# Kernel optimization log

Hardware: AMD Instinct MI355X
Metric: run time of the kernel (lower is better)

The kernel has to match this reference:

```python
import jax, jax.numpy as jnp
import numpy as np

B, S, D, H = 4, 2048, 1024, 16
DK = D // H
SCALE = 1.0 / np.float32(np.sqrt(DK))


def setup_inputs() -> dict:
    key = jax.random.key(0)
    ks = jax.random.split(key, 11)
    w = lambda k: (jax.random.normal(k, (D, D), jnp.float32) * 0.02)
    b = lambda k: (jax.random.normal(k, (D,), jnp.float32) * 0.02)
    return {
        "Q": jax.random.normal(ks[0], (B, S, D), jnp.float32),
        "K": jax.random.normal(ks[1], (B, S, D), jnp.float32),
        "V": jax.random.normal(ks[2], (B, S, D), jnp.float32),
        "Wq": w(ks[3]), "bq": b(ks[4]),
        "Wk": w(ks[5]), "bk": b(ks[6]),
        "Wv": w(ks[7]), "bv": b(ks[8]),
        "Wo": w(ks[9]), "bo": b(ks[10]),
        # causal mask, broadcast over batch and heads: [1,1,S,S]
        "mask": jnp.tril(jnp.ones((1, 1, S, S), dtype=bool)),
    }


def reference(Q, K, V, Wq, bq, Wk, bk, Wv, bv, Wo, bo, mask):
    def proj(x, W, bias):
        # [B,S,D] -> [B,H,S,DK]
        return (x @ W + bias).reshape(B, S, H, DK).transpose(0, 2, 1, 3)

    q = proj(Q, Wq, bq)
    k = proj(K, Wk, bk)
    v = proj(V, Wv, bv)
    scores = jnp.einsum("bhqd,bhkd->bhqk", q, k) * SCALE  # [B,H,S,S]
    scores = jnp.where(mask, scores, jnp.float32(-1e9))
    attn = jax.nn.softmax(scores, axis=-1)
    out = jnp.einsum("bhqk,bhkd->bhqd", attn, v)  # [B,H,S,DK]
    out = out.transpose(0, 2, 1, 3).reshape(B, S, D)
    return out @ Wo + bo
```

## Files before the change

kernel.cpp:

```cpp
#include <hip/hip_runtime.h>
#include <hip/hip_bf16.h>
#include <stdint.h>

#define BB 4
#define SS 2048
#define DD 1024
#define HH 16
#define DKK 64
#define MM (BB * SS)

typedef __hip_bfloat16 bf16;
typedef __attribute__((ext_vector_type(8))) short frag8;
typedef __attribute__((ext_vector_type(4))) float f32x4;

#define GLDS16(g, l)                                                        \
  __builtin_amdgcn_global_load_lds(                                         \
      (const __attribute__((address_space(1))) void*)(g),                   \
      (__attribute__((address_space(3))) void*)(l), 16, 0, 0)

#define MFMA __builtin_amdgcn_mfma_f32_16x16x32_bf16

__device__ __forceinline__ unsigned short f2bu(float f) {
  __hip_bfloat16 h = __float2bfloat16(f);
  return *reinterpret_cast<unsigned short*>(&h);
}

struct WtArgs {
  const float* s[3];
  unsigned short* d[3];
};
__global__ __launch_bounds__(256) void wtrans_kernel(WtArgs a) {
  const float* __restrict__ W = a.s[blockIdx.z];
  unsigned short* __restrict__ Wt = a.d[blockIdx.z];
  __shared__ float t[64][68];
  const int n0 = blockIdx.x * 64, k0 = blockIdx.y * 64;
  const int tid = threadIdx.x;
#pragma unroll
  for (int it = 0; it < 4; ++it) {
    const int kk = it * 16 + (tid >> 4);
    const int nn = (tid & 15) * 4;
    const float4 v = *(const float4*)&W[(size_t)(k0 + kk) * DD + n0 + nn];
    *(float4*)&t[kk][nn] = v;
  }
  __syncthreads();
#pragma unroll
  for (int it = 0; it < 2; ++it) {
    const int n = it * 32 + (tid >> 3);
    const int c = tid & 7;
    frag8 pk;
#pragma unroll
    for (int j = 0; j < 8; ++j) pk[j] = (short)f2bu(t[c * 8 + j][n]);
    *(frag8*)&Wt[(size_t)(n0 + n) * DD + k0 + c * 8] = pk;
  }
}

struct CvtArgs {
  const float* s[3];
  unsigned short* d[3];
};
__global__ __launch_bounds__(256) void cvt_kernel(CvtArgs a) {
  const float* __restrict__ src = a.s[blockIdx.y];
  unsigned short* __restrict__ dst = a.d[blockIdx.y];
  const size_t i = ((size_t)blockIdx.x * 256 + threadIdx.x) * 8;
  const float4 v0 = *(const float4*)&src[i];
  const float4 v1 = *(const float4*)&src[i + 4];
  frag8 pk;
  pk[0] = (short)f2bu(v0.x); pk[1] = (short)f2bu(v0.y);
  pk[2] = (short)f2bu(v0.z); pk[3] = (short)f2bu(v0.w);
  pk[4] = (short)f2bu(v1.x); pk[5] = (short)f2bu(v1.y);
  pk[6] = (short)f2bu(v1.z); pk[7] = (short)f2bu(v1.w);
  *(frag8*)&dst[i] = pk;
}

struct GArgs {
  const void* A[3];
  const unsigned short* W[3];
  const float* bias[3];
  void* out[3];
  float oscale[3];
  int abf16[3];
  int omode[3];
};

__global__ __launch_bounds__(256) void gemm32_kernel(GArgs ga) {
  constexpr int K = DD;
  const int z = blockIdx.z;
  const unsigned short* __restrict__ A = (const unsigned short*)ga.A[z];
  const unsigned short* __restrict__ Wt = ga.W[z];
  const float* __restrict__ bias = ga.bias[z];
  void* __restrict__ outv = ga.out[z];
  const float oscale = ga.oscale[z];
  const int omode = ga.omode[z];

  __shared__ unsigned short As[2][128 * 32];
  __shared__ unsigned short Bs[2][128 * 32];
  const int tid = threadIdx.x;
  const int wave = tid >> 6, lane = tid & 63, quad = lane >> 4, l15 = lane & 15;
  const int wr = wave >> 1, wc = wave & 1;
  const int mt = blockIdx.x * 8 + (blockIdx.y >> 3);
  const int nt = blockIdx.y & 7;
  const int m0 = mt * 128, n0 = nt * 128;

  f32x4 acc[4][4] = {};

  auto stage = [&](int buf, int k0) {
#pragma unroll
    for (int j = 0; j < 2; ++j) {
      const int win = wave * 2 + j;
      const int srl = lane >> 3;
      const int pp = lane & 7;
      const int p = pp ^ srl;
      const int row = (win * 8 + srl) * 2 + (p >> 2);
      const int c = p & 3;
      const unsigned off = __builtin_amdgcn_readfirstlane(
          (unsigned)(buf * 8192 + win * 1024));
      GLDS16(&A[(size_t)(m0 + row) * K + k0 + c * 8], (char*)&As[0][0] + off);
      GLDS16(&Wt[(size_t)(n0 + row) * K + k0 + c * 8], (char*)&Bs[0][0] + off);
    }
  };
  auto compute = [&](int buf) {
    frag8 af[4], bfr[4];
#pragma unroll
    for (int mi = 0; mi < 4; ++mi) {
      const int R = wr * 64 + mi * 16 + l15;
      const int sr = R >> 1;
      const int pp = (((R & 1) << 2) | quad) ^ (sr & 7);
      af[mi] = *(const frag8*)&As[buf][sr * 64 + pp * 8];
    }
#pragma unroll
    for (int ni = 0; ni < 4; ++ni) {
      const int R = wc * 64 + ni * 16 + l15;
      const int sr = R >> 1;
      const int pp = (((R & 1) << 2) | quad) ^ (sr & 7);
      bfr[ni] = *(const frag8*)&Bs[buf][sr * 64 + pp * 8];
    }
#pragma unroll
    for (int mi = 0; mi < 4; ++mi)
#pragma unroll
      for (int ni = 0; ni < 4; ++ni)
        acc[mi][ni] = MFMA(af[mi], bfr[ni], acc[mi][ni], 0, 0, 0);
  };

  stage(0, 0);
  __syncthreads();
#pragma unroll 1
  for (int t = 0; t < 32; ++t) {
    if (t + 1 < 32) stage((t & 1) ^ 1, (t + 1) * 32);
    compute(t & 1);
    __syncthreads();
  }

#pragma unroll
  for (int mi = 0; mi < 4; ++mi) {
#pragma unroll
    for (int ni = 0; ni < 4; ++ni) {
#pragma unroll
      for (int r = 0; r < 4; ++r) {
        const int grow = m0 + wr * 64 + mi * 16 + quad * 4 + r;
        const int gcol = n0 + wc * 64 + ni * 16 + l15;
        const float val = (acc[mi][ni][r] + bias[gcol]) * oscale;
        if (omode == 2) {
          ((float*)outv)[(size_t)grow * DD + gcol] = val;
        } else {
          const int b = grow / SS, s = grow % SS;
          const int h = gcol / DKK, dk = gcol % DKK;
          unsigned short* outp = (unsigned short*)outv;
          if (omode == 0)
            outp[(((size_t)(b * HH + h)) * SS + s) * DKK + dk] = f2bu(val);
          else
            outp[(((size_t)(b * HH + h)) * DKK + dk) * SS + s] = f2bu(val);
        }
      }
    }
  }
}

__global__ __launch_bounds__(256) void gemm_kernel(GArgs ga) {
  constexpr int K = DD;
  const int z = blockIdx.z;
  const void* __restrict__ Av = ga.A[z];
  const unsigned short* __restrict__ Wt = ga.W[z];
  const float* __restrict__ bias = ga.bias[z];
  void* __restrict__ outv = ga.out[z];
  const float oscale = ga.oscale[z];
  const int abf = ga.abf16[z];
  const int omode = ga.omode[z];

  __shared__ unsigned short Bs[2][128 * 64];
  __shared__ unsigned short As[2][128 * 64];
  const int tid = threadIdx.x;
  const int wave = tid >> 6, lane = tid & 63, quad = lane >> 4, l15 = lane & 15;
  const int wr = wave >> 1, wc = wave & 1;
  const int mt = blockIdx.x * 8 + (blockIdx.y >> 3);
  const int nt = blockIdx.y & 7;
  const int m0 = mt * 128, n0 = nt * 128;

  f32x4 acc[4][4] = {};
  float4 r0[4], r1[4];

  auto stageB = [&](int buf, int k0) {
#pragma unroll
    for (int c = 0; c < 4; ++c) {
      const int row = c * 32 + wave * 8 + (lane >> 3);
      const int gc = ((lane & 7) ^ (row & 7)) * 8;
      const unsigned short* g = &Wt[(size_t)(n0 + row) * K + k0 + gc];
      unsigned off = __builtin_amdgcn_readfirstlane(
          (unsigned)(buf * 16384 + (c * 32 + wave * 8) * 128));
      GLDS16(g, (char*)&Bs[0][0] + off);
    }
  };
  auto stageA16 = [&](int buf, int k0) {
    const unsigned short* Ap = (const unsigned short*)Av;
#pragma unroll
    for (int c = 0; c < 4; ++c) {
      const int row = c * 32 + wave * 8 + (lane >> 3);
      const int gc = ((lane & 7) ^ (row & 7)) * 8;
      const unsigned short* g = &Ap[(size_t)(m0 + row) * K + k0 + gc];
      unsigned off = __builtin_amdgcn_readfirstlane(
          (unsigned)(buf * 16384 + (c * 32 + wave * 8) * 128));
      GLDS16(g, (char*)&As[0][0] + off);
    }
  };
  auto loadA32 = [&](int k0) {
    const float* Ap = (const float*)Av;
#pragma unroll
    for (int it = 0; it < 4; ++it) {
      const int row = it * 32 + (tid >> 3);
      const int c = tid & 7;
      r0[it] = *(const float4*)&Ap[(size_t)(m0 + row) * K + k0 + c * 8];
      r1[it] = *(const float4*)&Ap[(size_t)(m0 + row) * K + k0 + c * 8 + 4];
    }
  };
  auto writeA32 = [&](int buf) {
#pragma unroll
    for (int it = 0; it < 4; ++it) {
      const int row = it * 32 + (tid >> 3);
      const int c = tid & 7;
      frag8 pk;
      pk[0] = (short)f2bu(r0[it].x); pk[1] = (short)f2bu(r0[it].y);
      pk[2] = (short)f2bu(r0[it].z); pk[3] = (short)f2bu(r0[it].w);
      pk[4] = (short)f2bu(r1[it].x); pk[5] = (short)f2bu(r1[it].y);
      pk[6] = (short)f2bu(r1[it].z); pk[7] = (short)f2bu(r1[it].w);
      *(frag8*)&As[buf][row * 64 + ((c ^ (row & 7)) * 8)] = pk;
    }
  };
  auto compute = [&](int buf) {
#pragma unroll
    for (int s = 0; s < 2; ++s) {
      frag8 a2[4], b2[4];
#pragma unroll
      for (int mi = 0; mi < 4; ++mi)
        a2[mi] = *(const frag8*)&As[buf][(wr * 64 + mi * 16 + l15) * 64 +
                                         (((s * 4 + quad) ^ (l15 & 7)) * 8)];
#pragma unroll
      for (int ni = 0; ni < 4; ++ni)
        b2[ni] = *(const frag8*)&Bs[buf][(wc * 64 + ni * 16 + l15) * 64 +
                                         (((s * 4 + quad) ^ (l15 & 7)) * 8)];
#pragma unroll
      for (int mi = 0; mi < 4; ++mi)
#pragma unroll
        for (int ni = 0; ni < 4; ++ni)
          acc[mi][ni] = MFMA(a2[mi], b2[ni], acc[mi][ni], 0, 0, 0);
    }
  };

  if (abf) {
    stageB(0, 0);
    stageA16(0, 0);
  } else {
    loadA32(0);
    stageB(0, 0);
    writeA32(0);
  }
  __syncthreads();

#pragma unroll 1
  for (int t = 0; t < 16; t += 2) {
    if (t + 1 < 16) {
      if (abf) {
        stageB(1, (t + 1) * 64);
        stageA16(1, (t + 1) * 64);
      } else {
        loadA32((t + 1) * 64);
        stageB(1, (t + 1) * 64);
      }
    }
    compute(0);
    if (!abf && t + 1 < 16) writeA32(1);
    __syncthreads();
    if (t + 2 < 16) {
      if (abf) {
        stageB(0, (t + 2) * 64);
        stageA16(0, (t + 2) * 64);
      } else {
        loadA32((t + 2) * 64);
        stageB(0, (t + 2) * 64);
      }
    }
    compute(1);
    if (!abf && t + 2 < 16) writeA32(0);
    __syncthreads();
  }

#pragma unroll
  for (int mi = 0; mi < 4; ++mi) {
#pragma unroll
    for (int ni = 0; ni < 4; ++ni) {
#pragma unroll
      for (int r = 0; r < 4; ++r) {
        const int grow = m0 + wr * 64 + mi * 16 + quad * 4 + r;
        const int gcol = n0 + wc * 64 + ni * 16 + l15;
        const float val = (acc[mi][ni][r] + bias[gcol]) * oscale;
        if (omode == 2) {
          ((float*)outv)[(size_t)grow * DD + gcol] = val;
        } else {
          const int b = grow / SS, s = grow % SS;
          const int h = gcol / DKK, dk = gcol % DKK;
          unsigned short* outp = (unsigned short*)outv;
          if (omode == 0)
            outp[(((size_t)(b * HH + h)) * SS + s) * DKK + dk] = f2bu(val);
          else
            outp[(((size_t)(b * HH + h)) * DKK + dk) * SS + s] = f2bu(val);
        }
      }
    }
  }
}

__global__ __launch_bounds__(512) void fattn_kernel(
    const unsigned short* __restrict__ q, const unsigned short* __restrict__ k,
    const unsigned short* __restrict__ vt, unsigned short* __restrict__ ctx) {
  __shared__ unsigned short Ks[2][64 * 64];
  __shared__ unsigned short Vs[2][64 * 64];
  __shared__ unsigned short P_lds[8][16][36];
  const int tid = threadIdx.x;
  const int wave = tid >> 6, lane = tid & 63, quad = lane >> 4, l15 = lane & 15;
  const int bh = blockIdx.x & 63;
  const int tp = blockIdx.x >> 6;
  const size_t qkb = (size_t)bh * SS * DKK;
  const size_t vtb = (size_t)bh * DKK * SS;
  const int b = bh / HH, h = bh % HH;

  frag8 ones;
#pragma unroll
  for (int s = 0; s < 8; ++s) ones[s] = (short)0x3F80;

  auto stage = [&](int buf, int jt) {
    const int row = wave * 8 + (lane >> 3);
    const int gc = ((lane & 7) ^ (lane >> 3)) * 8;
    const unsigned off =
        __builtin_amdgcn_readfirstlane((unsigned)(buf * 8192 + wave * 1024));
    GLDS16(&k[qkb + (size_t)(jt * 64 + row) * DKK + gc],
           (char*)&Ks[0][0] + off);
    GLDS16(&vt[vtb + (size_t)row * SS + jt * 64 + gc], (char*)&Vs[0][0] + off);
  };

  for (int half = 0; half < 2; ++half) {
    const int t = half ? (15 - tp) : tp;
    const int q0 = t * 128 + wave * 16;

    const frag8 aq0 =
        *(const frag8*)&q[qkb + (size_t)(q0 + l15) * DKK + quad * 8];
    const frag8 aq1 =
        *(const frag8*)&q[qkb + (size_t)(q0 + l15) * DKK + 32 + quad * 8];

    f32x4 oacc[4] = {};
    f32x4 lacc = {};

    const int nT = 2 * t + 2;
    stage(0, 0);
    __syncthreads();

    for (int jt = 0; jt < nT; ++jt) {
      const int p = jt & 1;
      if (jt + 1 < nT) stage(1 - p, jt + 1);
      const bool allmask = jt * 64 > q0 + 15;
      const bool anymask = jt * 64 + 63 > q0;

      if (!allmask) {
#pragma unroll
        for (int jsub = 0; jsub < 2; ++jsub) {
          f32x4 sc[2];
#pragma unroll
          for (int g = 0; g < 2; ++g) {
            const int row = jsub * 32 + g * 16 + l15;
            const frag8 kf0 =
                *(const frag8*)&Ks[p][row * 64 + ((quad ^ (l15 & 7)) * 8)];
            const frag8 kf1 =
                *(const frag8*)&Ks[p][row * 64 + (((4 + quad) ^ (l15 & 7)) * 8)];
            f32x4 z = {};
            z = MFMA(aq0, kf0, z, 0, 0, 0);
            sc[g] = MFMA(aq1, kf1, z, 0, 0, 0);
          }
          float p0[4], p1[4];
          if (anymask) {
            const int jg = jt * 64 + jsub * 32;
#pragma unroll
            for (int r = 0; r < 4; ++r) {
              const int ig = q0 + quad * 4 + r;
              p0[r] = (jg + l15 <= ig) ? __expf(sc[0][r]) : 0.f;
              p1[r] = (jg + 16 + l15 <= ig) ? __expf(sc[1][r]) : 0.f;
            }
          } else {
#pragma unroll
            for (int r = 0; r < 4; ++r) {
              p0[r] = __expf(sc[0][r]);
              p1[r] = __expf(sc[1][r]);
            }
          }
#pragma unroll
          for (int r = 0; r < 4; ++r) {
            P_lds[wave][quad * 4 + r][l15] = f2bu(p0[r]);
            P_lds[wave][quad * 4 + r][16 + l15] = f2bu(p1[r]);
          }
          const frag8 pa = *(const frag8*)&P_lds[wave][l15][quad * 8];
#pragma unroll
          for (int c = 0; c < 4; ++c) {
            const int vrow = c * 16 + l15;
            const int chunk = ((jsub * 4 + quad) ^ (l15 & 7));
            const frag8 vf = *(const frag8*)&Vs[p][vrow * 64 + chunk * 8];
            oacc[c] = MFMA(pa, vf, oacc[c], 0, 0, 0);
          }
          lacc = MFMA(pa, ones, lacc, 0, 0, 0);
        }
      }
      __syncthreads();
    }

#pragma unroll
    for (int r = 0; r < 4; ++r) {
      const float inv = 1.f / lacc[r];
      const int ig = q0 + quad * 4 + r;
#pragma unroll
      for (int c = 0; c < 4; ++c)
        ctx[((size_t)(b * SS + ig)) * DD + h * DKK + c * 16 + l15] =
            f2bu(oacc[c][r] * inv);
    }
  }
}

extern "C" void kernel_launch(void* const* d_in, const int* in_sizes, int n_in,
                              void* d_out, int out_size, void* d_ws,
                              size_t ws_size, hipStream_t stream) {
  const float* Q = (const float*)d_in[0];
  const float* K = (const float*)d_in[1];
  const float* V = (const float*)d_in[2];
  const float* Wq = (const float*)d_in[3];
  const float* bq = (const float*)d_in[4];
  const float* Wk = (const float*)d_in[5];
  const float* bk = (const float*)d_in[6];
  const float* Wv = (const float*)d_in[7];
  const float* bv = (const float*)d_in[8];
  const float* Wo = (const float*)d_in[9];
  const float* bo = (const float*)d_in[10];

  const size_t NE = (size_t)MM * DD;
  unsigned short* ctx = (unsigned short*)d_ws;
  unsigned short* qp = ctx + NE;
  unsigned short* kp = qp + NE;
  unsigned short* vtp = kp + NE;
  unsigned short* Qb = vtp + NE;
  unsigned short* Kb = Qb + NE;
  unsigned short* Vb = Kb + NE;
  unsigned short* Wqt = ctx;
  unsigned short* Wkt = ctx + 1048576;
  unsigned short* Wvt = ctx + 2097152;
  unsigned short* Wot = qp;

  const bool fastQK = ws_size >= (size_t)6 * NE * sizeof(unsigned short);
  const bool fastV = ws_size >= (size_t)7 * NE * sizeof(unsigned short);

  WtArgs wa1;
  wa1.s[0] = Wq; wa1.s[1] = Wk; wa1.s[2] = Wv;
  wa1.d[0] = Wqt; wa1.d[1] = Wkt; wa1.d[2] = Wvt;
  wtrans_kernel<<<dim3(16, 16, 3), 256, 0, stream>>>(wa1);

  CvtArgs ca;
  if (fastQK) {
    int ncvt = 2;
    ca.s[0] = Q; ca.d[0] = Qb;
    ca.s[1] = K; ca.d[1] = Kb;
    if (fastV) { ca.s[2] = V; ca.d[2] = Vb; ncvt = 3; }
    cvt_kernel<<<dim3(NE / 2048, ncvt), 256, 0, stream>>>(ca);
  }

  GArgs g3;
  g3.A[0] = fastQK ? (const void*)Qb : (const void*)Q;
  g3.A[1] = fastQK ? (const void*)Kb : (const void*)K;
  g3.A[2] = fastV ? (const void*)Vb : (const void*)V;
  g3.W[0] = Wqt; g3.W[1] = Wkt; g3.W[2] = Wvt;
  g3.bias[0] = bq; g3.bias[1] = bk; g3.bias[2] = bv;
  g3.out[0] = qp; g3.out[1] = kp; g3.out[2] = vtp;
  g3.oscale[0] = 0.125f; g3.oscale[1] = 1.f; g3.oscale[2] = 1.f;
  g3.abf16[0] = fastQK ? 1 : 0; g3.abf16[1] = fastQK ? 1 : 0;
  g3.abf16[2] = fastV ? 1 : 0;
  g3.omode[0] = 0; g3.omode[1] = 0; g3.omode[2] = 1;
  if (fastV) {
    gemm32_kernel<<<dim3(8, 64, 3), 256, 0, stream>>>(g3);
  } else {
    gemm_kernel<<<dim3(8, 64, 3), 256, 0, stream>>>(g3);
  }

  fattn_kernel<<<dim3(BB * HH * 8), 512, 0, stream>>>(qp, kp, vtp, ctx);

  WtArgs wa2;
  wa2.s[0] = Wo; wa2.d[0] = Wot;
  wa2.s[1] = Wo; wa2.d[1] = Wot;
  wa2.s[2] = Wo; wa2.d[2] = Wot;
  wtrans_kernel<<<dim3(16, 16, 1), 256, 0, stream>>>(wa2);

  GArgs go;
  go.A[0] = (const void*)ctx; go.W[0] = Wot; go.bias[0] = bo;
  go.out[0] = (void*)d_out; go.oscale[0] = 1.f;
  go.abf16[0] = 1; go.omode[0] = 2;
  go.A[1] = go.A[0]; go.W[1] = go.W[0]; go.bias[1] = go.bias[0];
  go.out[1] = go.out[0]; go.oscale[1] = 1.f; go.abf16[1] = 1; go.omode[1] = 2;
  go.A[2] = go.A[0]; go.W[2] = go.W[0]; go.bias[2] = go.bias[0];
  go.out[2] = go.out[0]; go.oscale[2] = 1.f; go.abf16[2] = 1; go.omode[2] = 2;
  if (fastV) {
    gemm32_kernel<<<dim3(8, 64, 1), 256, 0, stream>>>(go);
  } else {
    gemm_kernel<<<dim3(8, 64, 1), 256, 0, stream>>>(go);
  }
}
```

Measured before the change: 356.0 us.

## Triple-buffer GEMM loads with vmcnt waits and shrink attention query tiles

The projection GEMM moves from double to triple-buffered LDS staging. It issues loads two tiles ahead and uses explicit s_waitcnt vmcnt plus raw s_barrier, so the global-to-LDS latency is hidden longer. The attention kernel is reworked to 64-row query tiles with 4 waves per block and twice as many blocks. This removes idle fully-masked waves on diagonal tiles and improves load balance, at the cost of more K/V reloads per query row and more LDS for the GEMM.

Result: no change. 362.8 us (+1.9%).

```diff
diff --git a/kernel.cpp b/kernel.cpp
--- a/kernel.cpp
+++ b/kernel.cpp
@@ -19,6 +19,8 @@
       (__attribute__((address_space(3))) void*)(l), 16, 0, 0)
 
 #define MFMA __builtin_amdgcn_mfma_f32_16x16x32_bf16
+#define SBAR asm volatile("s_barrier" ::: "memory")
+#define WAITN(n) asm volatile("s_waitcnt vmcnt(" #n ")" ::: "memory")
 
 __device__ __forceinline__ unsigned short f2bu(float f) {
   __hip_bfloat16 h = __float2bfloat16(f);
@@ -92,8 +94,8 @@
   const float oscale = ga.oscale[z];
   const int omode = ga.omode[z];
 
-  __shared__ unsigned short As[2][128 * 32];
-  __shared__ unsigned short Bs[2][128 * 32];
+  __shared__ unsigned short As[3][128 * 32];
+  __shared__ unsigned short Bs[3][128 * 32];
   const int tid = threadIdx.x;
   const int wave = tid >> 6, lane = tid & 63, quad = lane >> 4, l15 = lane & 15;
   const int wr = wave >> 1, wc = wave & 1;
@@ -142,12 +144,20 @@
   };
 
   stage(0, 0);
-  __syncthreads();
+  stage(1, 32);
+  WAITN(4);
+  SBAR;
+
 #pragma unroll 1
   for (int t = 0; t < 32; ++t) {
-    if (t + 1 < 32) stage((t & 1) ^ 1, (t + 1) * 32);
-    compute(t & 1);
-    __syncthreads();
+    if (t + 2 < 32) stage((t + 2) % 3, (t + 2) * 32);
+    compute(t % 3);
+    if (t + 2 < 32) {
+      WAITN(4);
+    } else if (t + 1 < 32) {
+      WAITN(0);
+    }
+    SBAR;
   }
 
 #pragma unroll
@@ -327,12 +337,12 @@
   }
 }
 
-__global__ __launch_bounds__(512) void fattn_kernel(
+__global__ __launch_bounds__(256) void fattn_kernel(
     const unsigned short* __restrict__ q, const unsigned short* __restrict__ k,
     const unsigned short* __restrict__ vt, unsigned short* __restrict__ ctx) {
   __shared__ unsigned short Ks[2][64 * 64];
   __shared__ unsigned short Vs[2][64 * 64];
-  __shared__ unsigned short P_lds[8][16][36];
+  __shared__ unsigned short P_lds[4][16][36];
   const int tid = threadIdx.x;
   const int wave = tid >> 6, lane = tid & 63, quad = lane >> 4, l15 = lane & 15;
   const int bh = blockIdx.x & 63;
@@ -346,18 +356,29 @@
   for (int s = 0; s < 8; ++s) ones[s] = (short)0x3F80;
 
   auto stage = [&](int buf, int jt) {
-    const int row = wave * 8 + (lane >> 3);
-    const int gc = ((lane & 7) ^ (lane >> 3)) * 8;
-    const unsigned off =
-        __builtin_amdgcn_readfirstlane((unsigned)(buf * 8192 + wave * 1024));
-    GLDS16(&k[qkb + (size_t)(jt * 64 + row) * DKK + gc],
-           (char*)&Ks[0][0] + off);
-    GLDS16(&vt[vtb + (size_t)row * SS + jt * 64 + gc], (char*)&Vs[0][0] + off);
+#pragma unroll
+    for (int c = 0; c < 2; ++c) {
+      const int row = wave * 16 + c * 8 + (lane >> 3);
+      const int gc = ((lane & 7) ^ (row & 7)) * 8;
+      const unsigned short* g = &k[qkb + (size_t)(jt * 64 + row) * DKK + gc];
+      unsigned off = __builtin_amdgcn_readfirstlane(
+          (unsigned)(buf * 8192 + (wave * 16 + c * 8) * 128));
+      GLDS16(g, (char*)&Ks[0][0] + off);
+    }
+#pragma unroll
+    for (int c = 0; c < 2; ++c) {
+      const int row = wave * 16 + c * 8 + (lane >> 3);
+      const int gc = ((lane & 7) ^ (row & 7)) * 8;
+      const unsigned short* g = &vt[vtb + (size_t)row * SS + jt * 64 + gc];
+      unsigned off = __builtin_amdgcn_readfirstlane(
+          (unsigned)(buf * 8192 + (wave * 16 + c * 8) * 128));
+      GLDS16(g, (char*)&Vs[0][0] + off);
+    }
   };
 
   for (int half = 0; half < 2; ++half) {
-    const int t = half ? (15 - tp) : tp;
-    const int q0 = t * 128 + wave * 16;
+    const int t = half ? (31 - tp) : tp;
+    const int q0 = t * 64 + wave * 16;
 
     const frag8 aq0 =
         *(const frag8*)&q[qkb + (size_t)(q0 + l15) * DKK + quad * 8];
@@ -367,62 +388,59 @@
     f32x4 oacc[4] = {};
     f32x4 lacc = {};
 
-    const int nT = 2 * t + 2;
+    const int nT = t + 1;
     stage(0, 0);
     __syncthreads();
 
     for (int jt = 0; jt < nT; ++jt) {
       const int p = jt & 1;
       if (jt + 1 < nT) stage(1 - p, jt + 1);
-      const bool allmask = jt * 64 > q0 + 15;
-      const bool anymask = jt * 64 + 63 > q0;
-
-      if (!allmask) {
-#pragma unroll
-        for (int jsub = 0; jsub < 2; ++jsub) {
-          f32x4 sc[2];
-#pragma unroll
-          for (int g = 0; g < 2; ++g) {
-            const int row = jsub * 32 + g * 16 + l15;
-            const frag8 kf0 =
-                *(const frag8*)&Ks[p][row * 64 + ((quad ^ (l15 & 7)) * 8)];
-            const frag8 kf1 =
-                *(const frag8*)&Ks[p][row * 64 + (((4 + quad) ^ (l15 & 7)) * 8)];
-            f32x4 z = {};
-            z = MFMA(aq0, kf0, z, 0, 0, 0);
-            sc[g] = MFMA(aq1, kf1, z, 0, 0, 0);
+      const bool diag = (jt == t);
+
+#pragma unroll
+      for (int jsub = 0; jsub < 2; ++jsub) {
+        f32x4 sc[2];
+#pragma unroll
+        for (int g = 0; g < 2; ++g) {
+          const int row = jsub * 32 + g * 16 + l15;
+          const frag8 kf0 =
+              *(const frag8*)&Ks[p][row * 64 + ((quad ^ (l15 & 7)) * 8)];
+          const frag8 kf1 =
+              *(const frag8*)&Ks[p][row * 64 + (((4 + quad) ^ (l15 & 7)) * 8)];
+          f32x4 z = {};
+          z = MFMA(aq0, kf0, z, 0, 0, 0);
+          sc[g] = MFMA(aq1, kf1, z, 0, 0, 0);
+        }
+        float p0[4], p1[4];
+        if (diag) {
+          const int jg = jt * 64 + jsub * 32;
+#pragma unroll
+          for (int r = 0; r < 4; ++r) {
+            const int ig = q0 + quad * 4 + r;
+            p0[r] = (jg + l15 <= ig) ? __expf(sc[0][r]) : 0.f;
+            p1[r] = (jg + 16 + l15 <= ig) ? __expf(sc[1][r]) : 0.f;
           }
-          float p0[4], p1[4];
-          if (anymask) {
-            const int jg = jt * 64 + jsub * 32;
-#pragma unroll
-            for (int r = 0; r < 4; ++r) {
-              const int ig = q0 + quad * 4 + r;
-              p0[r] = (jg + l15 <= ig) ? __expf(sc[0][r]) : 0.f;
-              p1[r] = (jg + 16 + l15 <= ig) ? __expf(sc[1][r]) : 0.f;
-            }
-          } else {
-#pragma unroll
-            for (int r = 0; r < 4; ++r) {
-              p0[r] = __expf(sc[0][r]);
-              p1[r] = __expf(sc[1][r]);
-            }
+        } else {
+#pragma unroll
+          for (int r = 0; r < 4; ++r) {
+            p0[r] = __expf(sc[0][r]);
+            p1[r] = __expf(sc[1][r]);
           }
-#pragma unroll
-          for (int r = 0; r < 4; ++r) {
-            P_lds[wave][quad * 4 + r][l15] = f2bu(p0[r]);
-            P_lds[wave][quad * 4 + r][16 + l15] = f2bu(p1[r]);
-          }
-          const frag8 pa = *(const frag8*)&P_lds[wave][l15][quad * 8];
-#pragma unroll
-          for (int c = 0; c < 4; ++c) {
-            const int vrow = c * 16 + l15;
-            const int chunk = ((jsub * 4 + quad) ^ (l15 & 7));
-            const frag8 vf = *(const frag8*)&Vs[p][vrow * 64 + chunk * 8];
-            oacc[c] = MFMA(pa, vf, oacc[c], 0, 0, 0);
-          }
-          lacc = MFMA(pa, ones, lacc, 0, 0, 0);
         }
+#pragma unroll
+        for (int r = 0; r < 4; ++r) {
+          P_lds[wave][quad * 4 + r][l15] = f2bu(p0[r]);
+          P_lds[wave][quad * 4 + r][16 + l15] = f2bu(p1[r]);
+        }
+        const frag8 pa = *(const frag8*)&P_lds[wave][l15][quad * 8];
+#pragma unroll
+        for (int c = 0; c < 4; ++c) {
+          const int vrow = c * 16 + l15;
+          const int chunk = ((jsub * 4 + quad) ^ (l15 & 7));
+          const frag8 vf = *(const frag8*)&Vs[p][vrow * 64 + chunk * 8];
+          oacc[c] = MFMA(pa, vf, oacc[c], 0, 0, 0);
+        }
+        lacc = MFMA(pa, ones, lacc, 0, 0, 0);
       }
       __syncthreads();
     }
@@ -501,7 +519,7 @@
     gemm_kernel<<<dim3(8, 64, 3), 256, 0, stream>>>(g3);
   }
 
-  fattn_kernel<<<dim3(BB * HH * 8), 512, 0, stream>>>(qp, kp, vtp, ctx);
+  fattn_kernel<<<dim3(BB * HH * 16), 256, 0, stream>>>(qp, kp, vtp, ctx);
 
   WtArgs wa2;
   wa2.s[0] = Wo; wa2.d[0] = Wot;
```
